# Optimization experiments

Hardware: AMD Instinct MI355X
Metric: run time of the kernel (lower is better)

The kernel has to match this reference:

```python
import jax, jax.numpy as jnp
import numpy as np

D_MODEL = 1024
N_HEADS = 16
HEAD_DIM = D_MODEL // N_HEADS
WINDOW = 256
N_GLOBAL = 2
EPS = 1e-5


def _layernorm(x, g, b):
    mu = jnp.mean(x, axis=-1, keepdims=True)
    var = jnp.var(x, axis=-1, keepdims=True)
    return (x - mu) * jax.lax.rsqrt(var + EPS) * g + b


def _longformer_mask(T):
    i = jnp.arange(T)[:, None]
    j = jnp.arange(T)[None, :]
    half = WINDOW // 2
    local = (j >= i - half) & (j <= i + half)
    glob = jnp.zeros((T, T), dtype=bool)
    if N_GLOBAL >= 1:
        glob = glob | (i == 0) | (j == 0)
    if N_GLOBAL >= 2 and T > 1:
        glob = glob | (i == T - 1) | (j == T - 1)
    allowed = (local | glob) & (j <= i)  # causal
    neg_inf = jnp.float32(-jnp.inf)
    return jnp.where(allowed, jnp.float32(0.0), neg_inf)[None, None]  # (1,1,T,T)


def setup_inputs() -> dict:
    key = jax.random.key(0)
    ks = jax.random.split(key, 8)
    B, T, D = 2, 2048, D_MODEL
    s = 0.02
    return {
        "x": jax.random.normal(ks[0], (B, T, D), dtype=jnp.float32),
        "ln1_g": jnp.ones((D,), jnp.float32),
        "ln1_b": jnp.zeros((D,), jnp.float32),
        "ln2_g": jnp.ones((D,), jnp.float32),
        "ln2_b": jnp.zeros((D,), jnp.float32),
        "Wq": jax.random.normal(ks[1], (D, D), jnp.float32) * s,
        "Wk": jax.random.normal(ks[2], (D, D), jnp.float32) * s,
        "Wv": jax.random.normal(ks[3], (D, D), jnp.float32) * s,
        "Wo": jax.random.normal(ks[4], (D, D), jnp.float32) * s,
        "bo": jnp.zeros((D,), jnp.float32),
        "W1": jax.random.normal(ks[5], (D, 4 * D), jnp.float32) * s,
        "b1": jnp.zeros((4 * D,), jnp.float32),
        "W2": jax.random.normal(ks[6], (4 * D, D), jnp.float32) * s,
        "b2": jnp.zeros((D,), jnp.float32),
    }


def reference(x, ln1_g, ln1_b, ln2_g, ln2_b, Wq, Wk, Wv, Wo, bo, W1, b1, W2, b2):
    B, T, D = x.shape
    h = _layernorm(x, ln1_g, ln1_b)
    # (B,T,D) -> (B,H,T,hd)
    q = (h @ Wq).reshape(B, T, N_HEADS, HEAD_DIM).transpose(0, 2, 1, 3)
    k = (h @ Wk).reshape(B, T, N_HEADS, HEAD_DIM).transpose(0, 2, 1, 3)
    v = (h @ Wv).reshape(B, T, N_HEADS, HEAD_DIM).transpose(0, 2, 1, 3)
    mask = _longformer_mask(T)
    scores = jnp.einsum("bhqd,bhkd->bhqk", q, k) / np.sqrt(HEAD_DIM) + mask
    attn = jax.nn.softmax(scores, axis=-1)
    out = jnp.einsum("bhqk,bhkd->bhqd", attn, v)
    out = out.transpose(0, 2, 1, 3).reshape(B, T, D)
    x = x + out @ Wo + bo
    h2 = _layernorm(x, ln2_g, ln2_b)
    ffn = jax.nn.gelu(h2 @ W1 + b1, approximate=False) @ W2 + b2
    return x + ffn
```

## Files before the change

### kernel.cpp

```cpp
#include <hip/hip_runtime.h>
#include <cmath>

#define Tseq 2048
#define Dm   1024
#define NHd  16
#define HDim 64
#define Mrows 4096
#define QS   3072
#define PAD  72
#define NSPLIT 16

typedef _Float16 f16;
typedef _Float16 half8 __attribute__((ext_vector_type(8)));
typedef _Float16 half4 __attribute__((ext_vector_type(4)));
typedef float    floatx4 __attribute__((ext_vector_type(4)));

#define ASYNC_COPY16(g, l)                                                       \
  __builtin_amdgcn_global_load_lds((const __attribute__((address_space(1))) void*)(g), \
                                   (__attribute__((address_space(3))) void*)(l), 16, 0, 0)

#define SBAR()                                    \
  do {                                            \
    asm volatile("" ::: "memory");                \
    __builtin_amdgcn_s_barrier();                 \
    asm volatile("" ::: "memory");                \
  } while (0)

#define STAGE4(gptr, ldsbase)                                                    \
  do {                                                                           \
    _Pragma("unroll")                                                            \
    for (int i_ = 0; i_ < 4; ++i_)                                               \
      ASYNC_COPY16((gptr) + (size_t)(i_ * 64) * Kd, (ldsbase) + i_ * 4096 + ldsW); \
  } while (0)

__device__ __forceinline__ float gelu_f(float v) {
  const float u = 0.7978845608028654f * (v + 0.044715f * v * v * v);
  const float e = __expf(2.0f * u);
  return 0.5f * v * (2.0f - 2.0f / (e + 1.0f));
}

__global__ __launch_bounds__(256) void transp_f16(const float* __restrict__ W,
                                                  f16* __restrict__ Wt, int K, int N) {
  __shared__ float tile[32][33];
  const int n0 = blockIdx.x * 32, k0 = blockIdx.y * 32;
  const int tx = threadIdx.x & 31, ty = threadIdx.x >> 5;
#pragma unroll
  for (int i = 0; i < 32; i += 8)
    tile[ty + i][tx] = W[(size_t)(k0 + ty + i) * N + n0 + tx];
  __syncthreads();
#pragma unroll
  for (int i = 0; i < 32; i += 8)
    Wt[(size_t)(n0 + ty + i) * K + k0 + tx] = (f16)tile[tx][ty + i];
}

__global__ __launch_bounds__(256) void transp_qkv(const float* __restrict__ Wq,
                                                  const float* __restrict__ Wk,
                                                  const float* __restrict__ Wv,
                                                  f16* __restrict__ Wt) {
  __shared__ float tile[32][33];
  const float* W = (blockIdx.z == 0) ? Wq : (blockIdx.z == 1) ? Wk : Wv;
  f16* dst = Wt + (size_t)blockIdx.z * Dm * Dm;
  const int n0 = blockIdx.x * 32, k0 = blockIdx.y * 32;
  const int tx = threadIdx.x & 31, ty = threadIdx.x >> 5;
#pragma unroll
  for (int i = 0; i < 32; i += 8)
    tile[ty + i][tx] = W[(size_t)(k0 + ty + i) * Dm + n0 + tx];
  __syncthreads();
#pragma unroll
  for (int i = 0; i < 32; i += 8)
    dst[(size_t)(n0 + ty + i) * Dm + k0 + tx] = (f16)tile[tx][ty + i];
}

__global__ __launch_bounds__(256) void ln_f16(const float* __restrict__ x,
                                              const float* __restrict__ g,
                                              const float* __restrict__ bb,
                                              f16* __restrict__ out) {
  const int row = blockIdx.x, t = threadIdx.x;
  const float4 v = ((const float4*)(x + (size_t)row * Dm))[t];
  float s  = v.x + v.y + v.z + v.w;
  float ss = v.x * v.x + v.y * v.y + v.z * v.z + v.w * v.w;
#pragma unroll
  for (int m = 32; m >= 1; m >>= 1) { s += __shfl_xor(s, m); ss += __shfl_xor(ss, m); }
  __shared__ float red[8];
  if ((t & 63) == 0) { red[t >> 6] = s; red[4 + (t >> 6)] = ss; }
  __syncthreads();
  const float S  = red[0] + red[1] + red[2] + red[3];
  const float SS = red[4] + red[5] + red[6] + red[7];
  const float mean = S * (1.0f / Dm);
  const float inv  = rsqrtf(SS * (1.0f / Dm) - mean * mean + 1e-5f);
  const float4 gg = ((const float4*)g)[t];
  const float4 bv = ((const float4*)bb)[t];
  half4 o;
  o.x = (f16)(((v.x - mean) * inv) * gg.x + bv.x);
  o.y = (f16)(((v.y - mean) * inv) * gg.y + bv.y);
  o.z = (f16)(((v.z - mean) * inv) * gg.z + bv.z);
  o.w = (f16)(((v.w - mean) * inv) * gg.w + bv.w);
  *((half4*)(out + (size_t)row * Dm) + t) = o;
}

template <int NS>
__global__ __launch_bounds__(256) void reduce_ln(const f16* __restrict__ P,
                                                 const float* __restrict__ resid,
                                                 const float* __restrict__ bias,
                                                 const float* __restrict__ g,
                                                 const float* __restrict__ bb,
                                                 float* __restrict__ x1,
                                                 f16* __restrict__ h) {
  const int row = blockIdx.x, t = threadIdx.x;
  const size_t idx = (size_t)row * (Dm / 4) + t;
  const float4 r = ((const float4*)resid)[idx];
  const float4 b = ((const float4*)bias)[t];
  float4 o; o.x = r.x + b.x; o.y = r.y + b.y; o.z = r.z + b.z; o.w = r.w + b.w;
#pragma unroll
  for (int z = 0; z < NS; ++z) {
    const half4 p = ((const half4*)(P + (size_t)z * Mrows * Dm))[idx];
    o.x += (float)p[0]; o.y += (float)p[1]; o.z += (float)p[2]; o.w += (float)p[3];
  }
  ((float4*)x1)[idx] = o;
  float s  = o.x + o.y + o.z + o.w;
  float ss = o.x * o.x + o.y * o.y + o.z * o.z + o.w * o.w;
#pragma unroll
  for (int m = 32; m >= 1; m >>= 1) { s += __shfl_xor(s, m); ss += __shfl_xor(ss, m); }
  __shared__ float red[8];
  if ((t & 63) == 0) { red[t >> 6] = s; red[4 + (t >> 6)] = ss; }
  __syncthreads();
  const float S  = red[0] + red[1] + red[2] + red[3];
  const float SS = red[4] + red[5] + red[6] + red[7];
  const float mean = S * (1.0f / Dm);
  const float inv  = rsqrtf(SS * (1.0f / Dm) - mean * mean + 1e-5f);
  const float4 gg = ((const float4*)g)[t];
  const float4 bv = ((const float4*)bb)[t];
  half4 oh;
  oh[0] = (f16)(((o.x - mean) * inv) * gg.x + bv.x);
  oh[1] = (f16)(((o.y - mean) * inv) * gg.y + bv.y);
  oh[2] = (f16)(((o.z - mean) * inv) * gg.z + bv.z);
  oh[3] = (f16)(((o.w - mean) * inv) * gg.w + bv.w);
  ((half4*)h)[idx] = oh;
}

template <int NS>
__global__ __launch_bounds__(256) void reduceK(const f16* __restrict__ P,
                                               const float* __restrict__ resid,
                                               const float* __restrict__ bias,
                                               float* __restrict__ out) {
  const int t = blockIdx.x * 256 + threadIdx.x;
  const int col4 = t & (Dm / 4 - 1);
  const float4 r = ((const float4*)resid)[t];
  const float4 b = ((const float4*)bias)[col4];
  float4 o; o.x = r.x + b.x; o.y = r.y + b.y; o.z = r.z + b.z; o.w = r.w + b.w;
#pragma unroll
  for (int z = 0; z < NS; ++z) {
    const half4 p = ((const half4*)(P + (size_t)z * Mrows * Dm))[t];
    o.x += (float)p[0]; o.y += (float)p[1]; o.z += (float)p[2]; o.w += (float)p[3];
  }
  ((float4*)out)[t] = o;
}

template <int EPI, int LNZ>
__global__ __launch_bounds__(256, 4) void gemm_f16(const f16* __restrict__ A,
                                                   const f16* __restrict__ Bt,
                                                   int M, int N, int K, int kLen,
                                                   const float* __restrict__ bias,
                                                   f16* __restrict__ Ch) {
  constexpr int NZ = 1 << LNZ;
  __shared__ f16 As[128 * 64];
  __shared__ f16 Bs[128 * 64];
  const int tid = threadIdx.x;
  int bx, by, bz;
  if (EPI == 5) {
    const int lin = blockIdx.x;
    bz = lin & (NZ - 1);
    bx = (lin >> LNZ) & 7;
    by = lin >> (LNZ + 3);
  } else {
    bx = blockIdx.x; by = blockIdx.y; bz = 0;
  }
  const int m0 = by * 128, n0 = bx * 128;
  const int kOff = bz * kLen;
  const int w = tid >> 6, l = tid & 63;
  const int wr = (w >> 1) * 64, wc = (w & 1) * 64;
  const int c = l & 15, qq = l >> 4;
  const int cx = c & 7;
  const int srow = tid >> 3;
  const int scol = ((tid & 7) ^ (srow & 7)) * 8;

  floatx4 acc[4][4] = {};

  const f16* Ab = A + (size_t)(m0 + srow) * K + kOff + scol;
  const f16* Bb = Bt + (size_t)(n0 + srow) * K + kOff + scol;

  for (int k0 = 0; k0 < kLen; k0 += 64) {
    __syncthreads();
#pragma unroll
    for (int i = 0; i < 4; ++i) {
      ASYNC_COPY16(Ab + k0 + (size_t)(i * 32) * K, As + i * 2048 + w * 512);
      ASYNC_COPY16(Bb + k0 + (size_t)(i * 32) * K, Bs + i * 2048 + w * 512);
    }
    __syncthreads();
    half8 af[4][2], bfr[4][2];
#pragma unroll
    for (int t = 0; t < 4; ++t) {
      const int ra = (wr + t * 16 + c) * 64;
      af[t][0] = *(const half8*)&As[ra + ((qq ^ cx) * 8)];
      af[t][1] = *(const half8*)&As[ra + (((4 + qq) ^ cx) * 8)];
      const int rb = (wc + t * 16 + c) * 64;
      bfr[t][0] = *(const half8*)&Bs[rb + ((qq ^ cx) * 8)];
      bfr[t][1] = *(const half8*)&Bs[rb + (((4 + qq) ^ cx) * 8)];
    }
#pragma unroll
    for (int ti = 0; ti < 4; ++ti)
#pragma unroll
      for (int tj = 0; tj < 4; ++tj) {
        acc[ti][tj] = __builtin_amdgcn_mfma_f32_16x16x32_f16(af[ti][0], bfr[tj][0], acc[ti][tj], 0, 0, 0);
        acc[ti][tj] = __builtin_amdgcn_mfma_f32_16x16x32_f16(af[ti][1], bfr[tj][1], acc[ti][tj], 0, 0, 0);
      }
  }

  f16* Cw = (EPI == 5) ? (Ch + (size_t)bz * M * N) : Ch;
#pragma unroll
  for (int ti = 0; ti < 4; ++ti)
#pragma unroll
    for (int tj = 0; tj < 4; ++tj)
#pragma unroll
      for (int r = 0; r < 4; ++r) {
        const int row = m0 + wr + ti * 16 + qq * 4 + r;
        const int col = n0 + wc + tj * 16 + c;
        const size_t idx = (size_t)row * N + col;
        float v = acc[ti][tj][r];
        if (EPI == 2) {
          Cw[idx] = (f16)gelu_f(v + bias[col]);
        } else {
          Cw[idx] = (f16)v;
        }
      }
}

template <int EPI, int LNZ, int NT>
__global__ __launch_bounds__(512, 2) void gemm256(const f16* __restrict__ A,
                                                  const f16* __restrict__ Bt,
                                                  int M, int N, int Kd,
                                                  const float* __restrict__ bias,
                                                  f16* __restrict__ Ch) {
  __shared__ f16 As[2][256 * 64];
  __shared__ f16 Bs[2][256 * 64];

  const int nwg = gridDim.x;
  const int lin = blockIdx.x;
  const int q8 = nwg >> 3, r8 = nwg & 7;
  const int xcd = lin & 7, idx8 = lin >> 3;
  const int wgid = (xcd < r8 ? xcd * (q8 + 1) : r8 * (q8 + 1) + (xcd - r8) * q8) + idx8;
  int bz = 0, rest = wgid;
  if (EPI == 5) {
    const int zLen = nwg >> LNZ;
    bz = wgid / zLen;
    rest = wgid - bz * zLen;
  }
  const int nbx = N >> 8;
  const int bx = rest % nbx, by = rest / nbx;
  const int m0 = by << 8, n0 = bx << 8;
  const int kOff = bz * (NT * 64);

  const int tid = threadIdx.x;
  const int w = tid >> 6, l = tid & 63;
  const int c = l & 15, qq = l >> 4, cx = c & 7;
  const int wr = (w >> 2) << 7;
  const int wc = (w & 3) << 6;
  const int srow = tid >> 3;
  const int scol = ((tid & 7) ^ (srow & 7)) << 3;

  const f16* gA = A + (size_t)(m0 + srow) * Kd + kOff + scol;
  const f16* gB = Bt + (size_t)(n0 + srow) * Kd + kOff + scol;
  const int ldsW = (w << 3) * 64;

  floatx4 acc[8][4] = {};
  half8 aA[4], aB[4], aC[4], aD[4], b0[4], b1[4];

  auto LDA = [&](half8* dst, const f16* base, int mqb, int ks4) {
#pragma unroll
    for (int i = 0; i < 4; ++i)
      dst[i] = *(const half8*)&base[(wr + (mqb + i) * 16 + c) * 64 + (((ks4 + qq) ^ cx) << 3)];
  };
  auto LDB = [&](half8* dst, const f16* base, int ks4) {
#pragma unroll
    for (int i = 0; i < 4; ++i)
      dst[i] = *(const half8*)&base[(wc + i * 16 + c) * 64 + (((ks4 + qq) ^ cx) << 3)];
  };
  auto MM = [&](int mqb, half8* af, half8* bf) {
#pragma unroll
    for (int i = 0; i < 4; ++i)
#pragma unroll
      for (int nq = 0; nq < 4; ++nq)
        acc[mqb + i][nq] =
            __builtin_amdgcn_mfma_f32_16x16x32_f16(af[i], bf[nq], acc[mqb + i][nq], 0, 0, 0);
  };

  STAGE4(gA, &As[0][0]);
  STAGE4(gB, &Bs[0][0]);
  asm volatile("s_waitcnt vmcnt(0)" ::: "memory");
  SBAR();
  LDB(b0, &Bs[0][0], 0);
  LDA(aA, &As[0][0], 0, 0);

  for (int t = 0; t < NT; ++t) {
    const int cur = t & 1;
    const f16* Ac = &As[cur][0];
    const f16* Bc = &Bs[cur][0];
    f16* An = &As[cur ^ 1][0];
    f16* Bn = &Bs[cur ^ 1][0];
    const bool more = (t + 1 < NT);

    if (more) STAGE4(gB + (size_t)(t + 1) * 64, Bn);
    LDA(aB, Ac, 4, 0);
    SBAR();
    __builtin_amdgcn_s_setprio(1);
    MM(0, aA, b0);
    __builtin_amdgcn_s_setprio(0);
    SBAR();

    if (more) STAGE4(gA + (size_t)(t + 1) * 64, An);
    LDB(b1, Bc, 4);
    LDA(aC, Ac, 0, 4);
    SBAR();
    __builtin_amdgcn_s_setprio(1);
    MM(4, aB, b0);
    __builtin_amdgcn_s_setprio(0);
    SBAR();

    LDA(aD, Ac, 4, 4);
    SBAR();
    __builtin_amdgcn_s_setprio(1);
    MM(0, aC, b1);
    __builtin_amdgcn_s_setprio(0);
    if (more) asm volatile("s_waitcnt vmcnt(0)" ::: "memory");
    SBAR();

    if (more) {
      LDB(b0, Bn, 0);
      LDA(aA, An, 0, 0);
    }
    SBAR();
    __builtin_amdgcn_s_setprio(1);
    MM(4, aD, b1);
    __builtin_amdgcn_s_setprio(0);
    SBAR();
  }

  float bias_v[4] = {0.f, 0.f, 0.f, 0.f};
  if (EPI == 2) {
#pragma unroll
    for (int nq = 0; nq < 4; ++nq) bias_v[nq] = bias[n0 + wc + nq * 16 + c];
  }
  f16* Cw = (EPI == 5) ? (Ch + (size_t)bz * M * N) : Ch;
#pragma unroll
  for (int mq = 0; mq < 8; ++mq)
#pragma unroll
    for (int r = 0; r < 4; ++r) {
      const size_t rowb = (size_t)(m0 + wr + mq * 16 + qq * 4 + r) * N;
#pragma unroll
      for (int nq = 0; nq < 4; ++nq) {
        const int col = n0 + wc + nq * 16 + c;
        const float v = acc[mq][nq][r];
        if (EPI == 2) Cw[rowb + col] = (f16)gelu_f(v + bias_v[nq]);
        else          Cw[rowb + col] = (f16)v;
      }
    }
}

__global__ __launch_bounds__(256, 4) void attn_win(const f16* __restrict__ qkv,
                                                   f16* __restrict__ ao) {
  __shared__ f16 qs[64 * PAD];
  __shared__ f16 ks[64 * PAD];
  __shared__ f16 vts[64 * PAD];
  __shared__ f16 ps[64 * PAD];
  const int qt = blockIdx.x;
  const int b = blockIdx.y >> 4, hh = blockIdx.y & 15;
  const int q0 = qt * 64;
  const int tid = threadIdx.x, w = tid >> 6, l = tid & 63;
  const int c = l & 15, qq = l >> 4;
  const int wr = w * 16;
  const size_t base = ((size_t)b * Tseq) * QS + hh * HDim;
  const int rr = tid >> 2, ss = (tid & 3) * 16;

  {
    const f16* src = qkv + base + (size_t)(q0 + rr) * QS + ss;
    *(uint4*)&qs[rr * PAD + ss]     = *(const uint4*)src;
    *(uint4*)&qs[rr * PAD + ss + 8] = *(const uint4*)(src + 8);
  }

  float m_run[4], l_run[4];
  floatx4 oacc[4];
#pragma unroll
  for (int r = 0; r < 4; ++r) { m_run[r] = -INFINITY; l_run[r] = 0.f; }
#pragma unroll
  for (int td = 0; td < 4; ++td) oacc[td] = (floatx4){0.f, 0.f, 0.f, 0.f};

  int chunks[4]; int nch = 0;
  if (qt > 2) chunks[nch++] = 0;
  for (int ch = (qt - 2 > 0 ? qt - 2 : 0); ch <= qt; ++ch) chunks[nch++] = ch;

  for (int ci = 0; ci < nch; ++ci) {
    const int j0 = chunks[ci] * 64;
    __syncthreads();
    {
      const f16* srck = qkv + base + 1024 + (size_t)(j0 + rr) * QS + ss;
      *(uint4*)&ks[rr * PAD + ss]     = *(const uint4*)srck;
      *(uint4*)&ks[rr * PAD + ss + 8] = *(const uint4*)(srck + 8);
      const f16* srcv = qkv + base + 2048 + (size_t)(j0 + rr) * QS + ss;
      uint4 va0 = *(const uint4*)srcv;
      uint4 va1 = *(const uint4*)(srcv + 8);
      const f16* e0 = (const f16*)&va0;
      const f16* e1 = (const f16*)&va1;
#pragma unroll
      for (int i = 0; i < 8; ++i) vts[(ss + i) * PAD + rr] = e0[i];
#pragma unroll
      for (int i = 0; i < 8; ++i) vts[(ss + 8 + i) * PAD + rr] = e1[i];
    }
    __syncthreads();

    const half8 a0 = *(const half8*)&qs[(wr + c) * PAD + qq * 8];
    const half8 a1 = *(const half8*)&qs[(wr + c) * PAD + 32 + qq * 8];
    floatx4 sacc[4];
#pragma unroll
    for (int tj = 0; tj < 4; ++tj) {
      const half8 b0 = *(const half8*)&ks[(tj * 16 + c) * PAD + qq * 8];
      const half8 b1 = *(const half8*)&ks[(tj * 16 + c) * PAD + 32 + qq * 8];
      floatx4 s4 = {0.f, 0.f, 0.f, 0.f};
      s4 = __builtin_amdgcn_mfma_f32_16x16x32_f16(a0, b0, s4, 0, 0, 0);
      s4 = __builtin_amdgcn_mfma_f32_16x16x32_f16(a1, b1, s4, 0, 0, 0);
      sacc[tj] = s4;
    }

#pragma unroll
    for (int r = 0; r < 4; ++r) {
      const int ii = q0 + wr + qq * 4 + r;
      float sv[4];
      float mx = -INFINITY;
#pragma unroll
      for (int tj = 0; tj < 4; ++tj) {
        const int jj = j0 + tj * 16 + c;
        const bool allowed = (jj <= ii) && ((ii - jj) <= 128 || jj == 0);
        sv[tj] = allowed ? sacc[tj][r] * 0.125f : -INFINITY;
        mx = fmaxf(mx, sv[tj]);
      }
#pragma unroll
      for (int mm = 8; mm >= 1; mm >>= 1) mx = fmaxf(mx, __shfl_xor(mx, mm));
      const float mn = fmaxf(m_run[r], mx);
      const float alpha = (mn == -INFINITY) ? 1.f : __expf(m_run[r] - mn);
      float sum = 0.f;
      float p[4];
#pragma unroll
      for (int tj = 0; tj < 4; ++tj) { p[tj] = __expf(sv[tj] - mn); sum += p[tj]; }
#pragma unroll
      for (int mm = 8; mm >= 1; mm >>= 1) sum += __shfl_xor(sum, mm);
      l_run[r] = l_run[r] * alpha + sum;
      m_run[r] = mn;
#pragma unroll
      for (int td = 0; td < 4; ++td) oacc[td][r] *= alpha;
#pragma unroll
      for (int tj = 0; tj < 4; ++tj)
        ps[(wr + qq * 4 + r) * PAD + tj * 16 + c] = (f16)p[tj];
    }

    const half8 p0 = *(const half8*)&ps[(wr + c) * PAD + qq * 8];
    const half8 p1 = *(const half8*)&ps[(wr + c) * PAD + 32 + qq * 8];
#pragma unroll
    for (int td = 0; td < 4; ++td) {
      const half8 b0 = *(const half8*)&vts[(td * 16 + c) * PAD + qq * 8];
      const half8 b1 = *(const half8*)&vts[(td * 16 + c) * PAD + 32 + qq * 8];
      oacc[td] = __builtin_amdgcn_mfma_f32_16x16x32_f16(p0, b0, oacc[td], 0, 0, 0);
      oacc[td] = __builtin_amdgcn_mfma_f32_16x16x32_f16(p1, b1, oacc[td], 0, 0, 0);
    }
  }

#pragma unroll
  for (int td = 0; td < 4; ++td)
#pragma unroll
    for (int r = 0; r < 4; ++r) {
      const int ii = q0 + wr + qq * 4 + r;
      ao[((size_t)(b * Tseq + ii)) * Dm + hh * HDim + td * 16 + c] =
          (f16)(oacc[td][r] / l_run[r]);
    }
}

__global__ __launch_bounds__(256) void attn_row_part(const f16* __restrict__ qkv,
                                                     float* __restrict__ part) {
  const int bh = blockIdx.x, sp = blockIdx.y;
  const int b = bh >> 4, hh = bh & 15;
  const int tid = threadIdx.x;
  const size_t base = ((size_t)b * Tseq) * QS + hh * HDim;
  const int j0 = sp * (Tseq / NSPLIT);
  __shared__ float qsh[64];
  __shared__ float ps[128];
  __shared__ float red[4];
  __shared__ float red2[4];
  __shared__ float oacc[4][64];
  if (tid < 64) qsh[tid] = (float)qkv[base + (size_t)(Tseq - 1) * QS + tid] * 0.125f;
  __syncthreads();
  float sv = -INFINITY;
  if (tid < 128) {
    const f16* kr = qkv + base + 1024 + (size_t)(j0 + tid) * QS;
    float a0 = 0.f;
#pragma unroll
    for (int d8 = 0; d8 < 8; ++d8) {
      const half8 kv = *(const half8*)(kr + d8 * 8);
#pragma unroll
      for (int e = 0; e < 8; ++e) a0 = fmaf((float)kv[e], qsh[d8 * 8 + e], a0);
    }
    sv = a0;
  }
  float mx = sv;
#pragma unroll
  for (int mm = 32; mm >= 1; mm >>= 1) mx = fmaxf(mx, __shfl_xor(mx, mm));
  if ((tid & 63) == 0) red[tid >> 6] = mx;
  __syncthreads();
  const float M = fmaxf(red[0], red[1]);
  float p = 0.f;
  if (tid < 128) { p = __expf(sv - M); ps[tid] = p; }
  float sum = p;
#pragma unroll
  for (int mm = 32; mm >= 1; mm >>= 1) sum += __shfl_xor(sum, mm);
  if ((tid & 63) == 0) red2[tid >> 6] = sum;
  __syncthreads();
  const float L = red2[0] + red2[1];
  const int d = tid & 63, pt = tid >> 6;
  const f16* vb = qkv + base + 2048 + d;
  float acc = 0.f;
  for (int j = pt * 32; j < pt * 32 + 32; ++j)
    acc = fmaf(ps[j], (float)vb[(size_t)(j0 + j) * QS], acc);
  oacc[pt][d] = acc;
  __syncthreads();
  if (tid < 64) {
    const float o = oacc[0][tid] + oacc[1][tid] + oacc[2][tid] + oacc[3][tid];
    float* dst = part + ((size_t)bh * NSPLIT + sp) * 66;
    dst[tid] = o;
    if (tid == 0) { dst[64] = M; dst[65] = L; }
  }
}

__global__ __launch_bounds__(64) void attn_row_comb(const float* __restrict__ part,
                                                    f16* __restrict__ ao) {
  const int bh = blockIdx.x;
  const int b = bh >> 4, hh = bh & 15;
  const int tid = threadIdx.x;
  const float* pp = part + (size_t)bh * NSPLIT * 66;
  float M = -INFINITY;
#pragma unroll
  for (int s = 0; s < NSPLIT; ++s) M = fmaxf(M, pp[s * 66 + 64]);
  float L = 0.f, o = 0.f;
#pragma unroll
  for (int s = 0; s < NSPLIT; ++s) {
    const float wgt = __expf(pp[s * 66 + 64] - M);
    L += pp[s * 66 + 65] * wgt;
    o += pp[s * 66 + tid] * wgt;
  }
  ao[((size_t)(b * Tseq + Tseq - 1)) * Dm + hh * HDim + tid] = (f16)(o / L);
}

extern "C" void kernel_launch(void* const* d_in, const int* in_sizes, int n_in,
                              void* d_out, int out_size, void* d_ws, size_t ws_size,
                              hipStream_t stream) {
  (void)in_sizes; (void)n_in; (void)out_size; (void)ws_size;
  const float* x    = (const float*)d_in[0];
  const float* ln1g = (const float*)d_in[1];
  const float* ln1b = (const float*)d_in[2];
  const float* ln2g = (const float*)d_in[3];
  const float* ln2b = (const float*)d_in[4];
  const float* Wq   = (const float*)d_in[5];
  const float* Wk   = (const float*)d_in[6];
  const float* Wv   = (const float*)d_in[7];
  const float* Wo   = (const float*)d_in[8];
  const float* bo   = (const float*)d_in[9];
  const float* W1   = (const float*)d_in[10];
  const float* b1   = (const float*)d_in[11];
  const float* W2   = (const float*)d_in[12];
  const float* b2   = (const float*)d_in[13];
  float* out = (float*)d_out;

  char* w0 = (char*)d_ws;
  size_t off = 0;
  auto take = [&](size_t bytes) -> char* {
    char* p = w0 + off;
    off += (bytes + 255) & ~(size_t)255;
    return p;
  };
  f16*   WqkvT = (f16*)take((size_t)3 * Dm * Dm * 2);
  f16*   WoT   = (f16*)take((size_t)Dm * Dm * 2);
  f16*   W1T   = (f16*)take((size_t)Dm * 4 * Dm * 2);
  f16*   W2T   = (f16*)take((size_t)Dm * 4 * Dm * 2);
  f16*   hF    = (f16*)take((size_t)Mrows * Dm * 2);
  f16*   qkvh  = (f16*)take((size_t)Mrows * QS * 2);
  f16*   attnF = (f16*)take((size_t)Mrows * Dm * 2);
  float* x1    = (float*)take((size_t)Mrows * Dm * 4);
  f16*   h2F   = (f16*)take((size_t)Mrows * Dm * 2);
  f16*   pbuf  = (f16*)take((size_t)4 * Mrows * Dm * 2);
  float* rowp  = (float*)take((size_t)32 * NSPLIT * 66 * 4);
  f16*   ffn1F = qkvh;

  const dim3 blk(256);
  const dim3 blk512(512);
  transp_qkv<<<dim3(Dm / 32, Dm / 32, 3), blk, 0, stream>>>(Wq, Wk, Wv, WqkvT);
  transp_f16<<<dim3(Dm / 32, Dm / 32), blk, 0, stream>>>(Wo, WoT, Dm, Dm);
  transp_f16<<<dim3(4 * Dm / 32, Dm / 32), blk, 0, stream>>>(W1, W1T, Dm, 4 * Dm);
  transp_f16<<<dim3(Dm / 32, 4 * Dm / 32), blk, 0, stream>>>(W2, W2T, 4 * Dm, Dm);

  ln_f16<<<Mrows, blk, 0, stream>>>(x, ln1g, ln1b, hF);

  gemm256<3, 0, 16><<<dim3((Mrows / 256) * (QS / 256)), blk512, 0, stream>>>(
      hF, WqkvT, Mrows, QS, Dm, nullptr, qkvh);

  attn_row_part<<<dim3(2 * NHd, NSPLIT), blk, 0, stream>>>(qkvh, rowp);
  attn_win<<<dim3(Tseq / 64, 2 * NHd), blk, 0, stream>>>(qkvh, attnF);
  attn_row_comb<<<dim3(2 * NHd), dim3(64), 0, stream>>>(rowp, attnF);

  gemm_f16<5, 1><<<dim3(512), blk, 0, stream>>>(
      attnF, WoT, Mrows, Dm, Dm, Dm / 2, nullptr, pbuf);
  reduce_ln<2><<<Mrows, blk, 0, stream>>>(pbuf, x, bo, ln2g, ln2b, x1, h2F);

  gemm256<2, 0, 16><<<dim3((Mrows / 256) * (4 * Dm / 256)), blk512, 0, stream>>>(
      h2F, W1T, Mrows, 4 * Dm, Dm, b1, ffn1F);

  gemm256<5, 2, 16><<<dim3(4 * (Mrows / 256) * (Dm / 256)), blk512, 0, stream>>>(
      ffn1F, W2T, Mrows, Dm, 4 * Dm, nullptr, pbuf);
  reduceK<4><<<Mrows * Dm / 1024, blk, 0, stream>>>(pbuf, x1, b2, out);
}
```

Measured before the change: 347.5 us.

## Simplify gemm256 register pipeline and route QKV projection to 128-tile GEMM

Replaces the six-buffer fragment prefetch schedule in gemm256 with a two-buffer scheme. Each phase loads its A/B fragments from LDS right before its MFMA block, with explicit lgkmcnt waits and sched barriers. Both next-tile global-to-LDS copies are now issued at the start of each iteration. The QKV projection switches from gemm256 to the 128x128 gemm_f16 kernel, giving more blocks. This lowers register pressure and may raise occupancy, but the LDS reads are no longer hidden behind the MFMAs.

```diff
diff --git a/kernel.cpp b/kernel.cpp
--- a/kernel.cpp
+++ b/kernel.cpp
@@ -273,7 +273,7 @@
   const int ldsW = (w << 3) * 64;
 
   floatx4 acc[8][4] = {};
-  half8 aA[4], aB[4], aC[4], aD[4], b0[4], b1[4];
+  half8 aF[4], bF[4];
 
   auto LDA = [&](half8* dst, const f16* base, int mqb, int ks4) {
 #pragma unroll
@@ -298,8 +298,6 @@
   STAGE4(gB, &Bs[0][0]);
   asm volatile("s_waitcnt vmcnt(0)" ::: "memory");
   SBAR();
-  LDB(b0, &Bs[0][0], 0);
-  LDA(aA, &As[0][0], 0, 0);
 
   for (int t = 0; t < NT; ++t) {
     const int cur = t & 1;
@@ -309,39 +307,47 @@
     f16* Bn = &Bs[cur ^ 1][0];
     const bool more = (t + 1 < NT);
 
-    if (more) STAGE4(gB + (size_t)(t + 1) * 64, Bn);
-    LDA(aB, Ac, 4, 0);
-    SBAR();
+    LDA(aF, Ac, 0, 0);
+    LDB(bF, Bc, 0);
+    if (more) {
+      STAGE4(gA + (size_t)(t + 1) * 64, An);
+      STAGE4(gB + (size_t)(t + 1) * 64, Bn);
+    }
+    SBAR();
+    asm volatile("s_waitcnt lgkmcnt(0)" ::: "memory");
+    __builtin_amdgcn_sched_barrier(0);
     __builtin_amdgcn_s_setprio(1);
-    MM(0, aA, b0);
+    MM(0, aF, bF);
     __builtin_amdgcn_s_setprio(0);
     SBAR();
 
-    if (more) STAGE4(gA + (size_t)(t + 1) * 64, An);
-    LDB(b1, Bc, 4);
-    LDA(aC, Ac, 0, 4);
-    SBAR();
+    LDA(aF, Ac, 4, 0);
+    SBAR();
+    asm volatile("s_waitcnt lgkmcnt(0)" ::: "memory");
+    __builtin_amdgcn_sched_barrier(0);
     __builtin_amdgcn_s_setprio(1);
-    MM(4, aB, b0);
+    MM(4, aF, bF);
     __builtin_amdgcn_s_setprio(0);
     SBAR();
 
-    LDA(aD, Ac, 4, 4);
-    SBAR();
+    LDA(aF, Ac, 0, 4);
+    LDB(bF, Bc, 4);
+    SBAR();
+    asm volatile("s_waitcnt lgkmcnt(0)" ::: "memory");
+    __builtin_amdgcn_sched_barrier(0);
     __builtin_amdgcn_s_setprio(1);
-    MM(0, aC, b1);
+    MM(0, aF, bF);
+    __builtin_amdgcn_s_setprio(0);
+    SBAR();
+
+    LDA(aF, Ac, 4, 4);
+    SBAR();
+    asm volatile("s_waitcnt lgkmcnt(0)" ::: "memory");
+    __builtin_amdgcn_sched_barrier(0);
+    __builtin_amdgcn_s_setprio(1);
+    MM(4, aF, bF);
     __builtin_amdgcn_s_setprio(0);
     if (more) asm volatile("s_waitcnt vmcnt(0)" ::: "memory");
-    SBAR();
-
-    if (more) {
-      LDB(b0, Bn, 0);
-      LDA(aA, An, 0, 0);
-    }
-    SBAR();
-    __builtin_amdgcn_s_setprio(1);
-    MM(4, aD, b1);
-    __builtin_amdgcn_s_setprio(0);
     SBAR();
   }
 
@@ -605,8 +611,8 @@
 
   ln_f16<<<Mrows, blk, 0, stream>>>(x, ln1g, ln1b, hF);
 
-  gemm256<3, 0, 16><<<dim3((Mrows / 256) * (QS / 256)), blk512, 0, stream>>>(
-      hF, WqkvT, Mrows, QS, Dm, nullptr, qkvh);
+  gemm_f16<3, 0><<<dim3(QS / 128, Mrows / 128), blk, 0, stream>>>(
+      hF, WqkvT, Mrows, QS, Dm, Dm, nullptr, qkvh);
 
   attn_row_part<<<dim3(2 * NHd, NSPLIT), blk, 0, stream>>>(qkvh, rowp);
   attn_win<<<dim3(Tseq / 64, 2 * NHd), blk, 0, stream>>>(qkvh, attnF);
```

Result: no change. 347.5 us (+0.0%).
